# Optimization experiments

Hardware: AMD Instinct MI355X
Metric: run time of the kernel (lower is better)

The kernel has to match this reference:

```python
import jax, jax.numpy as jnp
import numpy as np

B, N, DIM, H = 4, 2048, 1024, 16
HEAD_DIM = DIM // H
SCALE = HEAD_DIM ** (-0.5)


def setup_inputs() -> dict:
    key = jax.random.key(0)
    k1, k2, k3 = jax.random.split(key, 3)
    x = jax.random.normal(k1, (B, N, DIM), dtype=jnp.float32)
    # nn.Linear(dim, 3*dim, bias=False): weight shape [3*dim, dim], y = x @ W.T
    w_qkv = jax.random.normal(k2, (3 * DIM, DIM), dtype=jnp.float32) * 0.02
    w_proj = jax.random.normal(k3, (DIM, DIM), dtype=jnp.float32) * 0.02
    return {"x": x, "w_qkv": w_qkv, "w_proj": w_proj}


def reference(x, w_qkv, w_proj):
    Bv, Nv, C = x.shape
    Dh = C // H
    # qkv projection -> [B, N, 3, H, Dh]
    qkv = (x @ w_qkv.T).reshape(Bv, Nv, 3, H, Dh)
    q, k, v = qkv[:, :, 0], qkv[:, :, 1], qkv[:, :, 2]  # each [B, N, H, Dh]
    # scaled dot-product attention per head (online-softmax loop collapses to this)
    scores = jnp.einsum("bnhd,bmhd->bhnm", q, k) * SCALE  # [B, H, N, N]
    attn = jax.nn.softmax(scores, axis=-1)
    out = jnp.einsum("bhnm,bmhd->bnhd", attn, v).reshape(Bv, Nv, C)
    return out @ w_proj.T
```

## Files before the change

### kernel.cpp

```cpp
#include <hip/hip_runtime.h>

typedef __bf16 bf16;
typedef bf16 bf16x8 __attribute__((ext_vector_type(8)));
typedef float f32x4 __attribute__((ext_vector_type(4)));
typedef float f32x16 __attribute__((ext_vector_type(16)));
typedef int i32x2 __attribute__((ext_vector_type(2)));

#define B_   4
#define N_   2048
#define DIM_ 1024
#define H_   16
#define DH_  64
#define M_   (B_ * N_)

#define CEXP 0.18033688f

#define GLOBAL_CP(g) (const __attribute__((address_space(1))) void*)(g)
#define LDS_CP(l)    (__attribute__((address_space(3))) void*)(l)

__global__ __launch_bounds__(256) void cvt_all(
    const float* __restrict__ x, const float* __restrict__ wq,
    const float* __restrict__ wp, bf16* __restrict__ o,
    int nx4, int nwq4, int nwp4)
{
    const int i = blockIdx.x * blockDim.x + threadIdx.x;
    const float* src; int si;
    if (i < nx4)                { src = x;  si = i; }
    else if (i < nx4 + nwq4)    { src = wq; si = i - nx4; }
    else                        { src = wp; si = i - nx4 - nwq4; }
    const float4 v = ((const float4*)src)[si];
    union { bf16 h[4]; uint2 u; } r;
    r.h[0] = (bf16)v.x; r.h[1] = (bf16)v.y;
    r.h[2] = (bf16)v.z; r.h[3] = (bf16)v.w;
    ((uint2*)o)[i] = r.u;
}

__global__ __launch_bounds__(256) void gemm_bt(
    const bf16* __restrict__ A, const bf16* __restrict__ Bm,
    int Ndim, int K, int mode,
    float* __restrict__ outf,
    bf16* __restrict__ qb, bf16* __restrict__ kbv, bf16* __restrict__ vbT)
{
    __shared__ bf16 As[128 * 64];
    __shared__ bf16 Bs[128 * 64];

    const int tid  = threadIdx.x;
    const int wave = tid >> 6;
    const int lane = tid & 63;
    const int quad = lane >> 4;
    const int lr   = lane & 15;
    const int wr   = wave >> 1, wc = wave & 1;
    const int m0 = blockIdx.y * 128;
    const int n0 = blockIdx.x * 128;

    f32x4 acc[4][4];
#pragma unroll
    for (int i = 0; i < 4; i++)
#pragma unroll
        for (int j = 0; j < 4; j++) acc[i][j] = f32x4{0.f, 0.f, 0.f, 0.f};

    const int sl8 = lane >> 3;
    const int sc8 = ((lane & 7) ^ (sl8 & 7)) * 8;

    for (int k0 = 0; k0 < K; k0 += 64) {
        __syncthreads();
#pragma unroll
        for (int c = 0; c < 4; c++) {
            const int ii  = wave * 4 + c;
            const int row = ii * 8 + sl8;
            __builtin_amdgcn_global_load_lds(
                GLOBAL_CP(A + (size_t)(m0 + row) * K + k0 + sc8),
                LDS_CP(&As[ii * 512 + lane * 8]), 16, 0, 0);
            __builtin_amdgcn_global_load_lds(
                GLOBAL_CP(Bm + (size_t)(n0 + row) * K + k0 + sc8),
                LDS_CP(&Bs[ii * 512 + lane * 8]), 16, 0, 0);
        }
        __syncthreads();

#pragma unroll
        for (int s = 0; s < 2; s++) {
            bf16x8 af[4], bfr[4];
#pragma unroll
            for (int i = 0; i < 4; i++) {
                const int R = wr * 64 + i * 16 + lr;
                af[i] = *(const bf16x8*)(&As[R * 64 + (((s * 4 + quad) ^ (R & 7)) << 3)]);
            }
#pragma unroll
            for (int j = 0; j < 4; j++) {
                const int R = wc * 64 + j * 16 + lr;
                bfr[j] = *(const bf16x8*)(&Bs[R * 64 + (((s * 4 + quad) ^ (R & 7)) << 3)]);
            }
#pragma unroll
            for (int i = 0; i < 4; i++)
#pragma unroll
                for (int j = 0; j < 4; j++)
                    acc[i][j] = __builtin_amdgcn_mfma_f32_16x16x32_bf16(
                        af[i], bfr[j], acc[i][j], 0, 0, 0);
        }
    }

#pragma unroll
    for (int i = 0; i < 4; i++) {
        const int mbase = m0 + wr * 64 + i * 16 + quad * 4;
#pragma unroll
        for (int j = 0; j < 4; j++) {
            const int n = n0 + wc * 64 + j * 16 + lr;
            if (mode == 0) {
#pragma unroll
                for (int r = 0; r < 4; r++)
                    outf[(size_t)(mbase + r) * Ndim + n] = acc[i][j][r];
            } else {
                const int which = n >> 10;
                const int h = (n >> 6) & 15;
                const int d = n & 63;
                const int b  = mbase >> 11;
                const int t0 = mbase & 2047;
                if (which == 2) {
                    union { uint2 u; bf16 hh[4]; } p;
#pragma unroll
                    for (int r = 0; r < 4; r++) p.hh[r] = (bf16)acc[i][j][r];
                    *(uint2*)(&vbT[(((size_t)(b * 16 + h)) * 64 + d) * 2048 + t0]) = p.u;
                } else {
                    bf16* dst = (which == 0) ? qb : kbv;
                    const float sc = (which == 0) ? CEXP : 1.0f;
#pragma unroll
                    for (int r = 0; r < 4; r++)
                        dst[(((size_t)(b * 16 + h)) * 2048 + t0 + r) * 64 + d] =
                            (bf16)(acc[i][j][r] * sc);
                }
            }
        }
    }
}

__global__ __launch_bounds__(256, 4) void attn_kernel(
    const bf16* __restrict__ qb, const bf16* __restrict__ kb,
    const bf16* __restrict__ vbT, bf16* __restrict__ ao)
{
    __shared__ bf16 Ks[2][32 * 128];
    __shared__ bf16 Vs[2][32 * 128];

    const int tid  = threadIdx.x;
    const int wave = tid >> 6;
    const int lane = tid & 63;
    const int l31  = lane & 31;
    const int hh   = lane >> 5;

    const int bid = blockIdx.x;
    const int qt  = (bid >> 3) & 15;
    const int bh  = ((bid >> 7) << 3) | (bid & 7);

    const bf16* Q  = qb  + (size_t)bh * N_ * DH_;
    const bf16* Kp = kb  + (size_t)bh * N_ * DH_;
    const bf16* Vp = vbT + (size_t)bh * DH_ * N_;

    bf16x8 qf[4];
#pragma unroll
    for (int ks = 0; ks < 4; ks++)
        qf[ks] = *(const bf16x8*)(Q + (size_t)(qt * 128 + wave * 32 + l31) * DH_
                                    + ks * 16 + hh * 8);

    f32x16 kZ;
#pragma unroll
    for (int r = 0; r < 16; r++) kZ[r] = 0.f;

    int kofs[8];
#pragma unroll
    for (int kbk = 0; kbk < 2; kbk++)
#pragma unroll
        for (int ks = 0; ks < 4; ks++) {
            const int R  = kbk * 32 + l31;
            const int rr = R >> 1;
            const int ch = ks * 2 + hh;
            const int pc = (((R & 1) << 3) | ch) ^ (rr & 15);
            kofs[kbk * 4 + ks] = rr * 256 + pc * 16;
        }
    int vofs[8];
#pragma unroll
    for (int kbk = 0; kbk < 2; kbk++)
#pragma unroll
        for (int dblk = 0; dblk < 2; dblk++)
#pragma unroll
            for (int half = 0; half < 2; half++) {
                const int Rv  = dblk * 32 + l31;
                const int rv  = Rv >> 1;
                const int chv = kbk * 4 + half * 2 + hh;
                const int pv_ = (((Rv & 1) << 3) | chv) ^ (rv & 15);
                vofs[kbk * 4 + dblk * 2 + half] = rv * 256 + pv_ * 16;
            }

    const int sr = lane >> 4;
    const int sp = lane & 15;
    const bf16* ksrc[2];
    const bf16* vsrc[2];
    int sdst[2];
#pragma unroll
    for (int c2 = 0; c2 < 2; c2++) {
        const int ii  = wave * 2 + c2;
        const int rr2 = ii * 4 + sr;
        const int lc  = sp ^ (rr2 & 15);
        const int kk  = 2 * rr2 + (lc >> 3);
        const int d0  = (lc & 7) * 8;
        ksrc[c2] = Kp + (size_t)kk * DH_ + d0;
        vsrc[c2] = Vp + (size_t)kk * N_ + d0;
        sdst[c2] = ii * 1024 + lane * 16;
    }

    const char* ksB = (const char*)Ks;
    const char* vsB = (const char*)Vs;
    char* ksBm = (char*)Ks;
    char* vsBm = (char*)Vs;

    f32x16 oacc[2];
#pragma unroll
    for (int r = 0; r < 16; r++) { oacc[0][r] = 0.f; oacc[1][r] = 0.f; }
    float lrow = 0.f;

#define STAGE()                                                               \
    {                                                                         \
        _Pragma("unroll")                                                     \
        for (int c2 = 0; c2 < 2; c2++) {                                      \
            __builtin_amdgcn_global_load_lds(GLOBAL_CP(ksrc[c2]),             \
                LDS_CP(ksBm + sdst[c2]), 16, 0, 0);                           \
            __builtin_amdgcn_global_load_lds(GLOBAL_CP(vsrc[c2]),             \
                LDS_CP(vsBm + sdst[c2]), 16, 0, 0);                           \
            ksrc[c2] += 64 * DH_;                 \
            vsrc[c2] += 64;                      \
            sdst[c2] ^= 8192;                           \
        }                                                                     \
    }

#define TILE(BUFB)                                                            \
    {                                                                         \
        float ssum = 0.f;                                                     \
        _Pragma("unroll")                                                     \
        for (int kbk = 0; kbk < 2; kbk++) {                                   \
            f32x16 e;                                                         \
            __builtin_amdgcn_s_setprio(1);                                    \
            _Pragma("unroll")                                                 \
            for (int ks = 0; ks < 4; ks++) {                                  \
                bf16x8 ak = *(const bf16x8*)(ksB + kofs[kbk * 4 + ks] + (BUFB)); \
                e = __builtin_amdgcn_mfma_f32_32x32x16_bf16(                  \
                        ak, qf[ks], ks == 0 ? kZ : e, 0, 0, 0);               \
            }                                                                 \
            __builtin_amdgcn_s_setprio(0);                                    \
            bf16x8 bv[2][2];                                                  \
            _Pragma("unroll")                                                 \
            for (int dblk = 0; dblk < 2; dblk++)                              \
                _Pragma("unroll")                                             \
                for (int half = 0; half < 2; half++)                          \
                    bv[dblk][half] = *(const bf16x8*)(                        \
                        vsB + vofs[kbk * 4 + dblk * 2 + half] + (BUFB));      \
            _Pragma("unroll")                                                 \
            for (int r = 0; r < 16; r++) e[r] = __builtin_amdgcn_exp2f(e[r]); \
            _Pragma("unroll")                                                 \
            for (int r = 0; r < 16; r++) ssum += e[r];                        \
            uint g[8];                                                        \
            _Pragma("unroll")                                                 \
            for (int m = 0; m < 8; m++) {                                     \
                union { uint u; bf16 h2[2]; } pk;                             \
                pk.h2[0] = (bf16)e[2 * m];                                    \
                pk.h2[1] = (bf16)e[2 * m + 1];                                \
                g[m] = pk.u;                                                  \
            }                                                                 \
            const i32x2 s0 = __builtin_amdgcn_permlane32_swap((int)g[0], (int)g[2], false, false); \
            const i32x2 s1 = __builtin_amdgcn_permlane32_swap((int)g[1], (int)g[3], false, false); \
            const i32x2 s2 = __builtin_amdgcn_permlane32_swap((int)g[4], (int)g[6], false, false); \
            const i32x2 s3 = __builtin_amdgcn_permlane32_swap((int)g[5], (int)g[7], false, false); \
            union { uint u[4]; bf16x8 v; } p0u, p1u;                          \
            p0u.u[0] = (uint)s0[0]; p0u.u[1] = (uint)s1[0];                   \
            p0u.u[2] = (uint)s0[1]; p0u.u[3] = (uint)s1[1];                   \
            p1u.u[0] = (uint)s2[0]; p1u.u[1] = (uint)s3[0];                   \
            p1u.u[2] = (uint)s2[1]; p1u.u[3] = (uint)s3[1];                   \
            __builtin_amdgcn_s_setprio(1);                                    \
            _Pragma("unroll")                                                 \
            for (int dblk = 0; dblk < 2; dblk++) {                            \
                oacc[dblk] = __builtin_amdgcn_mfma_f32_32x32x16_bf16(         \
                    p0u.v, bv[dblk][0], oacc[dblk], 0, 0, 0);                 \
                oacc[dblk] = __builtin_amdgcn_mfma_f32_32x32x16_bf16(         \
                    p1u.v, bv[dblk][1], oacc[dblk], 0, 0, 0);                 \
            }                                                                 \
            __builtin_amdgcn_s_setprio(0);                                    \
        }                                                                     \
        ssum += __shfl_xor(ssum, 32);                                         \
        lrow += ssum;                                                         \
    }

    STAGE();
    __syncthreads();

    for (int tt = 0; tt < 16; tt++) {
        STAGE();
        TILE(0);
        __syncthreads();
        if (tt < 15) STAGE();
        TILE(8192);
        __syncthreads();
    }
#undef STAGE
#undef TILE

    const int head = bh & 15;
    const int b    = bh >> 4;
    const float linv = 1.0f / lrow;
#pragma unroll
    for (int r = 0; r < 16; r++) {
        const int qr  = (r & 3) + 8 * (r >> 2) + 4 * hh;
        const float inv = __shfl(linv, qr);
        const int qrow = qt * 128 + wave * 32 + qr;
#pragma unroll
        for (int dblk = 0; dblk < 2; dblk++)
            ao[((size_t)(b * 2048 + qrow)) * 1024 + head * 64 + dblk * 32 + l31] =
                (bf16)(oacc[dblk][r] * inv);
    }
}

extern "C" void kernel_launch(void* const* d_in, const int* in_sizes, int n_in,
                              void* d_out, int out_size, void* d_ws, size_t ws_size,
                              hipStream_t stream)
{
    const float* x     = (const float*)d_in[0];
    const float* wqkv  = (const float*)d_in[1];
    const float* wproj = (const float*)d_in[2];
    float* out = (float*)d_out;

    const size_t nx  = (size_t)M_ * DIM_;
    const size_t nwq = (size_t)3 * DIM_ * DIM_;
    const size_t nwp = (size_t)DIM_ * DIM_;
    const size_t seg = (size_t)B_ * H_ * N_ * DH_;

    bf16* xb     = (bf16*)d_ws;
    bf16* wqkvb  = xb + nx;
    bf16* wprojb = wqkvb + nwq;
    bf16* qb     = wprojb + nwp;
    bf16* kb     = qb + seg;
    bf16* vbT    = kb + seg;
    bf16* ao     = xb;

    const int nx4  = (int)(nx / 4), nwq4 = (int)(nwq / 4), nwp4 = (int)(nwp / 4);
    cvt_all<<<(nx4 + nwq4 + nwp4) / 256, 256, 0, stream>>>(
        x, wqkv, wproj, xb, nx4, nwq4, nwp4);

    gemm_bt<<<dim3(24, 64), 256, 0, stream>>>(xb, wqkvb, 3 * DIM_, DIM_, 1,
                                              nullptr, qb, kb, vbT);
    attn_kernel<<<dim3(1024), 256, 0, stream>>>(qb, kb, vbT, ao);
    gemm_bt<<<dim3(8, 64), 256, 0, stream>>>(ao, wprojb, DIM_, DIM_, 0,
                                             out, nullptr, nullptr, nullptr);
}
```

Baseline: 275.5 us.

## Stage V tile transpose through LDS for coalesced vbT stores; retune attention occupancy

In the QKV GEMM epilogue, blocks that produce the V section now write their accumulator tile into shared memory with an XOR swizzle. They then read it back transposed and issue 16-byte coalesced stores into the transposed V layout, replacing the scattered 8-byte strided stores. Shared memory is merged into a single buffer so the staging can reuse it, and the Q/K path drops the per-element which-branch. Separately, the attention kernel's minimum blocks per CU drops from 4 to 3, and the zero accumulator is initialised per tile instead of being held in registers, which relaxes register pressure at the cost of occupancy.

Measured after the change: 273.8 us. No clear change (-0.6%).

```diff
diff --git a/kernel.cpp b/kernel.cpp
--- a/kernel.cpp
+++ b/kernel.cpp
@@ -41,8 +41,9 @@
     float* __restrict__ outf,
     bf16* __restrict__ qb, bf16* __restrict__ kbv, bf16* __restrict__ vbT)
 {
-    __shared__ bf16 As[128 * 64];
-    __shared__ bf16 Bs[128 * 64];
+    __shared__ bf16 smem[128 * 128];
+    bf16* As = smem;
+    bf16* Bs = smem + 128 * 64;
 
     const int tid  = threadIdx.x;
     const int wave = tid >> 6;
@@ -99,6 +100,39 @@
         }
     }
 
+    if (mode == 1 && blockIdx.x >= 16) {
+        __syncthreads();
+        const int b    = m0 >> 11;
+        const int t0_0 = m0 & 2047;
+        const int h0   = (n0 - 2048) >> 6;
+#pragma unroll
+        for (int i = 0; i < 4; i++) {
+            const int c8 = wr * 16 + i * 4 + quad;
+#pragma unroll
+            for (int j = 0; j < 4; j++) {
+                const int dl = wc * 64 + j * 16 + lr;
+                const int p8 = c8 ^ (lr << 1);
+                union { uint2 u; bf16 hh[4]; } p;
+#pragma unroll
+                for (int r = 0; r < 4; r++) p.hh[r] = (bf16)acc[i][j][r];
+                *(uint2*)((char*)smem + dl * 256 + p8 * 8) = p.u;
+            }
+        }
+        __syncthreads();
+#pragma unroll
+        for (int k = 0; k < 8; k++) {
+            const int cid = k * 256 + tid;
+            const int row = cid >> 4;
+            const int c16 = cid & 15;
+            const uint4 v = *(const uint4*)((const char*)smem
+                                + row * 256 + ((c16 ^ (row & 15)) * 16));
+            bf16* dst = vbT + ((size_t)(b * 16 + h0 + (row >> 6)) * 64
+                               + (row & 63)) * 2048 + t0_0 + c16 * 8;
+            *(uint4*)dst = v;
+        }
+        return;
+    }
+
 #pragma unroll
     for (int i = 0; i < 4; i++) {
         const int mbase = m0 + wr * 64 + i * 16 + quad * 4;
@@ -110,30 +144,22 @@
                 for (int r = 0; r < 4; r++)
                     outf[(size_t)(mbase + r) * Ndim + n] = acc[i][j][r];
             } else {
-                const int which = n >> 10;
                 const int h = (n >> 6) & 15;
                 const int d = n & 63;
                 const int b  = mbase >> 11;
                 const int t0 = mbase & 2047;
-                if (which == 2) {
-                    union { uint2 u; bf16 hh[4]; } p;
-#pragma unroll
-                    for (int r = 0; r < 4; r++) p.hh[r] = (bf16)acc[i][j][r];
-                    *(uint2*)(&vbT[(((size_t)(b * 16 + h)) * 64 + d) * 2048 + t0]) = p.u;
-                } else {
-                    bf16* dst = (which == 0) ? qb : kbv;
-                    const float sc = (which == 0) ? CEXP : 1.0f;
-#pragma unroll
-                    for (int r = 0; r < 4; r++)
-                        dst[(((size_t)(b * 16 + h)) * 2048 + t0 + r) * 64 + d] =
-                            (bf16)(acc[i][j][r] * sc);
-                }
+                bf16* dst = (n < 1024) ? qb : kbv;
+                const float sc = (n < 1024) ? CEXP : 1.0f;
+#pragma unroll
+                for (int r = 0; r < 4; r++)
+                    dst[(((size_t)(b * 16 + h)) * 2048 + t0 + r) * 64 + d] =
+                        (bf16)(acc[i][j][r] * sc);
             }
         }
     }
 }
 
-__global__ __launch_bounds__(256, 4) void attn_kernel(
+__global__ __launch_bounds__(256, 3) void attn_kernel(
     const bf16* __restrict__ qb, const bf16* __restrict__ kb,
     const bf16* __restrict__ vbT, bf16* __restrict__ ao)
 {
@@ -159,10 +185,6 @@
     for (int ks = 0; ks < 4; ks++)
         qf[ks] = *(const bf16x8*)(Q + (size_t)(qt * 128 + wave * 32 + l31) * DH_
                                     + ks * 16 + hh * 8);
-
-    f32x16 kZ;
-#pragma unroll
-    for (int r = 0; r < 16; r++) kZ[r] = 0.f;
 
     int kofs[8];
 #pragma unroll
@@ -236,12 +258,14 @@
         _Pragma("unroll")                                                     \
         for (int kbk = 0; kbk < 2; kbk++) {                                   \
             f32x16 e;                                                         \
+            _Pragma("unroll")                                                 \
+            for (int r = 0; r < 16; r++) e[r] = 0.f;                          \
             __builtin_amdgcn_s_setprio(1);                                    \
             _Pragma("unroll")                                                 \
             for (int ks = 0; ks < 4; ks++) {                                  \
                 bf16x8 ak = *(const bf16x8*)(ksB + kofs[kbk * 4 + ks] + (BUFB)); \
                 e = __builtin_amdgcn_mfma_f32_32x32x16_bf16(                  \
-                        ak, qf[ks], ks == 0 ? kZ : e, 0, 0, 0);               \
+                        ak, qf[ks], e, 0, 0, 0);                              \
             }                                                                 \
             __builtin_amdgcn_s_setprio(0);                                    \
             bf16x8 bv[2][2];                                                  \
```
